# Performance work log

Hardware: AMD Instinct MI355X
Metric: run time of the kernel (lower is better)

## Reference

```python
import jax, jax.numpy as jnp
import numpy as np

N_NODES = 50000
N_EDGES = 800000
IN_DIM = 96
OUT_DIM = 96
EDGE_DIM = 32
BN_EPS = 1e-5


def setup_inputs() -> dict:
    key = jax.random.key(0)
    ks = jax.random.split(key, 12)
    x = jax.random.normal(ks[0], (N_NODES, IN_DIM), dtype=jnp.float32)
    edge_index = jax.random.randint(ks[1], (2, N_EDGES), 0, N_NODES, dtype=jnp.int64)
    edge_attr = jax.random.normal(ks[2], (N_EDGES, EDGE_DIM), dtype=jnp.float32)
    # GINEConv edge projection Linear(edge_dim, in_dim)
    We = jax.random.normal(ks[3], (EDGE_DIM, IN_DIM), dtype=jnp.float32) / np.sqrt(EDGE_DIM)
    be = jnp.zeros((IN_DIM,), dtype=jnp.float32)
    # MLP: Linear(in_dim, out_dim) -> ReLU -> Linear(out_dim, out_dim)
    W1 = jax.random.normal(ks[4], (IN_DIM, OUT_DIM), dtype=jnp.float32) / np.sqrt(IN_DIM)
    b1 = jnp.zeros((OUT_DIM,), dtype=jnp.float32)
    W2 = jax.random.normal(ks[5], (OUT_DIM, OUT_DIM), dtype=jnp.float32) / np.sqrt(OUT_DIM)
    b2 = jnp.zeros((OUT_DIM,), dtype=jnp.float32)
    # BatchNorm1d affine params
    gamma = jnp.ones((OUT_DIM,), dtype=jnp.float32)
    beta = jnp.zeros((OUT_DIM,), dtype=jnp.float32)
    return {"x": x, "edge_index": edge_index, "edge_attr": edge_attr,
            "We": We, "be": be, "W1": W1, "b1": b1, "W2": W2, "b2": b2,
            "gamma": gamma, "beta": beta}


def reference(x, edge_index, edge_attr, We, be, W1, b1, W2, b2, gamma, beta):
    src = edge_index[0]  # x_j (message source)
    dst = edge_index[1]  # aggregation target
    # GINE message: ReLU(x_j + Lin(edge_attr)) per edge  [E, in_dim]
    msg = jax.nn.relu(x[src] + edge_attr @ We + be)
    # sum aggregation into dst nodes  [N, in_dim]
    aggr = jax.ops.segment_sum(msg, dst, num_segments=x.shape[0])
    # (1 + eps) * x + aggr, eps = 0 (GINEConv default)
    h = x + aggr
    # MLP: Linear -> ReLU -> Linear
    h = jax.nn.relu(h @ W1 + b1) @ W2 + b2
    # BatchNorm1d (training-mode batch statistics) + affine
    mean = jnp.mean(h, axis=0)
    var = jnp.mean(jnp.square(h - mean), axis=0)  # biased var, as torch BN uses
    h = (h - mean) * jax.lax.rsqrt(var + BN_EPS) * gamma + beta
    # ReLU (dropout is identity in eval / deterministic reference)
    return jax.nn.relu(h)
```

## Files before the change

### kernel.cpp

```cpp
#include <hip/hip_runtime.h>

typedef unsigned short ushort_t;
typedef unsigned int uint_t;
typedef __attribute__((ext_vector_type(8))) short bf16x8;
typedef __attribute__((ext_vector_type(4))) float f32x4;
typedef __attribute__((ext_vector_type(2))) float f32x2;

#define N_NODES 50000
#define N_EDGES 800000
#define BN_EPS 1e-5f

#define OFF_STATS 4800000
#define OFF_FLAG  4801536
#define NREP 8

#define SC_PAIR  0
#define SC_LEXCL 1600000
#define SC_DEG   1650016
#define SC_RANK  1700032
#define SC_BSUM  2500032

#define NB_SCAN 196
#define MTILE 64
#define NTILES ((N_NODES + MTILE - 1) / MTILE)

__device__ __forceinline__ ushort_t f2bf(float f) {
    uint_t u = __float_as_uint(f);
    uint_t r = ((u >> 16) & 1u) + 0x7fffu;
    return (ushort_t)((u + r) >> 16);
}

__global__ __launch_bounds__(256) void init_kernel(const int* __restrict__ ei,
                                                   int* __restrict__ flag,
                                                   int* __restrict__ deg,
                                                   float* __restrict__ stats) {
    const int gtid = blockIdx.x * 256 + threadIdx.x;
    const int nth = gridDim.x * 256;
    for (int i = gtid; i < N_NODES; i += nth) deg[i] = 0;
    if (gtid < NREP * 192) stats[gtid] = 0.f;
    if (blockIdx.x == 0) {
        __shared__ int s_any;
        if (threadIdx.x == 0) s_any = 0;
        __syncthreads();
        int nz = 0;
#pragma unroll
        for (int j = 0; j < 16; ++j) {
            const int p = 1 + 2 * (threadIdx.x * 16 + j) * 195;
            if (ei[p] != 0) nz = 1;
        }
        if (nz) atomicOr(&s_any, 1);
        __syncthreads();
        if (threadIdx.x == 0) *flag = s_any ? 0 : 1;
    }
}

__global__ __launch_bounds__(256) void hist_kernel(const int* __restrict__ ei,
                                                   const int* __restrict__ flag,
                                                   int* __restrict__ deg,
                                                   int* __restrict__ rank) {
    const int is64 = *flag;
    const int stride = gridDim.x * blockDim.x;
    for (int e = blockIdx.x * blockDim.x + threadIdx.x; e < N_EDGES; e += stride) {
        int s, d;
        if (is64) { s = ei[2 * e]; d = ei[2 * N_EDGES + 2 * e]; }
        else      { s = ei[e];     d = ei[N_EDGES + e]; }
        if ((uint_t)s < N_NODES && (uint_t)d < N_NODES)
            rank[e] = atomicAdd(&deg[d], 1);
    }
}

__global__ __launch_bounds__(256) void scanA_kernel(const int* __restrict__ deg,
                                                    int* __restrict__ lexcl,
                                                    int* __restrict__ bsum) {
    __shared__ int sd[256];
    const int tid = threadIdx.x;
    const int i = blockIdx.x * 256 + tid;
    const int v = (i < N_NODES) ? deg[i] : 0;
    sd[tid] = v;
    __syncthreads();
    for (int off = 1; off < 256; off <<= 1) {
        int u = (tid >= off) ? sd[tid - off] : 0;
        __syncthreads();
        sd[tid] += u;
        __syncthreads();
    }
    if (i < N_NODES) lexcl[i] = sd[tid] - v;
    if (tid == 255) bsum[blockIdx.x] = sd[255];
}

__device__ __forceinline__ void build_sbase(const int* __restrict__ bsum,
                                            int* sd, int* sbase, int* tot) {
    const int tid = threadIdx.x;
    const int v = (tid < NB_SCAN) ? bsum[tid] : 0;
    sd[tid] = v;
    __syncthreads();
    for (int off = 1; off < 256; off <<= 1) {
        int u = (tid >= off) ? sd[tid - off] : 0;
        __syncthreads();
        sd[tid] += u;
        __syncthreads();
    }
    if (tid < NB_SCAN) sbase[tid] = sd[tid] - v;
    if (tid == NB_SCAN - 1) *tot = sd[tid];
    __syncthreads();
}

__global__ __launch_bounds__(256) void scatter_kernel(const int* __restrict__ ei,
                                                      const int* __restrict__ flag,
                                                      const int* __restrict__ lexcl,
                                                      const int* __restrict__ bsum,
                                                      const int* __restrict__ rank,
                                                      int2* __restrict__ pair) {
    __shared__ int sd[256];
    __shared__ int sbase[NB_SCAN];
    __shared__ int tot;
    build_sbase(bsum, sd, sbase, &tot);

    const int is64 = *flag;
    const int stride = gridDim.x * blockDim.x;
    for (int e = blockIdx.x * blockDim.x + threadIdx.x; e < N_EDGES; e += stride) {
        int s, d;
        if (is64) { s = ei[2 * e]; d = ei[2 * N_EDGES + 2 * e]; }
        else      { s = ei[e];     d = ei[N_EDGES + e]; }
        if ((uint_t)s < N_NODES && (uint_t)d < N_NODES) {
            const int pos = sbase[d >> 8] + lexcl[d] + rank[e];
            pair[pos] = make_int2(e, s);
        }
    }
}

__global__ __launch_bounds__(256) void node_aggr_kernel(
    const float* __restrict__ x, const float* __restrict__ ea,
    const float* __restrict__ We, const float* __restrict__ be,
    const int2* __restrict__ pair, const int* __restrict__ lexcl,
    const int* __restrict__ bsum, float* __restrict__ hbuf,
    int n0, int n1) {
    __shared__ int sd[256];
    __shared__ int sbase[NB_SCAN];
    __shared__ int tot;
    build_sbase(bsum, sd, sbase, &tot);

    const int lane = threadIdx.x & 63;
    const int q = lane >> 4;
    const int t = lane & 15;
    const int wav = blockIdx.x * 4 + (threadIdx.x >> 6);
    const int nwav = gridDim.x * 4;

    bf16x8 Bf[6];
    float ben[6];
#pragma unroll
    for (int f = 0; f < 6; ++f) {
        const int n = t + 16 * f;
#pragma unroll
        for (int j = 0; j < 8; ++j) {
            const int k = q * 8 + j;
            Bf[f][j] = (short)f2bf(We[k * 96 + n]);
        }
        ben[f] = be[n];
    }

    for (int n = n0 + wav; n < n1; n += nwav) {
        const int off = sbase[n >> 8] + lexcl[n];
        const int offn = (n + 1 == N_NODES) ? tot
                         : sbase[(n + 1) >> 8] + lexcl[n + 1];
        const int deg = offn - off;

        float part[6];
#pragma unroll
        for (int f = 0; f < 6; ++f) part[f] = 0.f;

        for (int c0 = 0; c0 < deg; c0 += 16) {
            const int rem = deg - c0;
            int eid_t = -1, src_t = -1;
            if (t < rem) {
                const int2 p = pair[off + c0 + t];
                eid_t = p.x;
                src_t = p.y;
            }
            bf16x8 A = {0, 0, 0, 0, 0, 0, 0, 0};
            if (eid_t >= 0) {
                const float* row = ea + (size_t)eid_t * 32 + q * 8;
                f32x4 a0 = *(const f32x4*)(row);
                f32x4 a1 = *(const f32x4*)(row + 4);
#pragma unroll
                for (int j = 0; j < 4; ++j) {
                    A[j] = (short)f2bf(a0[j]);
                    A[4 + j] = (short)f2bf(a1[j]);
                }
            }

            f32x4 acc[6];
#pragma unroll
            for (int f = 0; f < 6; ++f) {
                f32x4 z = {0.f, 0.f, 0.f, 0.f};
                acc[f] = __builtin_amdgcn_mfma_f32_16x16x32_bf16(A, Bf[f], z, 0, 0, 0);
            }

            int s_r[4];
#pragma unroll
            for (int r = 0; r < 4; ++r) s_r[r] = __shfl(src_t, q * 4 + r);

#pragma unroll
            for (int r = 0; r < 4; ++r) {
                const int m = q * 4 + r;
                if (m < rem) {
                    const float* xrow = x + (size_t)s_r[r] * 96;
#pragma unroll
                    for (int f = 0; f < 6; ++f) {
                        float v = acc[f][r] + ben[f] + xrow[t + 16 * f];
                        part[f] += v > 0.f ? v : 0.f;
                    }
                }
            }
        }

#pragma unroll
        for (int f = 0; f < 6; ++f) {
            part[f] += __shfl_xor(part[f], 16);
            part[f] += __shfl_xor(part[f], 32);
        }

        if (q == 0) {
            const float* xn = x + (size_t)n * 96;
            float* hn = hbuf + (size_t)n * 96;
#pragma unroll
            for (int f = 0; f < 6; ++f) {
                const int col = t + 16 * f;
                hn[col] = part[f] + xn[col];
            }
        }
    }
}

__global__ __launch_bounds__(256) void mlp_kernel(
    float* buf, const float* __restrict__ W1g, const float* __restrict__ b1g,
    const float* __restrict__ W2g, const float* __restrict__ b2g,
    float* __restrict__ stats, int tb) {
    __shared__ float Ws[96 * 96];
    __shared__ float hsT[96][68];

    const int tid = threadIdx.x;
    const int fg = tid & 15;
    const int ng = tid >> 4;
    const int n0 = (tb + blockIdx.x) * MTILE;

    for (int i = tid; i < 96 * 96 / 4; i += 256)
        ((f32x4*)Ws)[i] = ((const f32x4*)W1g)[i];
    for (int i = tid; i < MTILE * 96 / 4; i += 256) {
        const int base = i * 4;
        const int nn = base / 96, k = base - nn * 96;
        f32x4 v = {0.f, 0.f, 0.f, 0.f};
        if (n0 + nn < N_NODES)
            v = *(const f32x4*)(buf + (size_t)(n0 + nn) * 96 + k);
        hsT[k][nn] = v[0]; hsT[k + 1][nn] = v[1];
        hsT[k + 2][nn] = v[2]; hsT[k + 3][nn] = v[3];
    }
    __syncthreads();

    float acc[4][6];
#pragma unroll
    for (int ff = 0; ff < 6; ++ff) {
        const float b = b1g[6 * fg + ff];
        acc[0][ff] = b; acc[1][ff] = b; acc[2][ff] = b; acc[3][ff] = b;
    }
    for (int k = 0; k < 96; ++k) {
        const f32x4 a = *(const f32x4*)&hsT[k][4 * ng];
        const float* wr = &Ws[k * 96 + 6 * fg];
        const f32x2 w01 = *(const f32x2*)(wr);
        const f32x2 w23 = *(const f32x2*)(wr + 2);
        const f32x2 w45 = *(const f32x2*)(wr + 4);
        const float w[6] = {w01[0], w01[1], w23[0], w23[1], w45[0], w45[1]};
#pragma unroll
        for (int nn = 0; nn < 4; ++nn)
#pragma unroll
            for (int ff = 0; ff < 6; ++ff) acc[nn][ff] += a[nn] * w[ff];
    }
    __syncthreads();

#pragma unroll
    for (int nn = 0; nn < 4; ++nn)
#pragma unroll
        for (int ff = 0; ff < 6; ++ff) {
            float v = acc[nn][ff];
            hsT[6 * fg + ff][4 * ng + nn] = v > 0.f ? v : 0.f;
        }
    for (int i = tid; i < 96 * 96 / 4; i += 256)
        ((f32x4*)Ws)[i] = ((const f32x4*)W2g)[i];
    __syncthreads();

#pragma unroll
    for (int ff = 0; ff < 6; ++ff) {
        const float b = b2g[6 * fg + ff];
        acc[0][ff] = b; acc[1][ff] = b; acc[2][ff] = b; acc[3][ff] = b;
    }
    for (int k = 0; k < 96; ++k) {
        const f32x4 a = *(const f32x4*)&hsT[k][4 * ng];
        const float* wr = &Ws[k * 96 + 6 * fg];
        const f32x2 w01 = *(const f32x2*)(wr);
        const f32x2 w23 = *(const f32x2*)(wr + 2);
        const f32x2 w45 = *(const f32x2*)(wr + 4);
        const float w[6] = {w01[0], w01[1], w23[0], w23[1], w45[0], w45[1]};
#pragma unroll
        for (int nn = 0; nn < 4; ++nn)
#pragma unroll
            for (int ff = 0; ff < 6; ++ff) acc[nn][ff] += a[nn] * w[ff];
    }

#pragma unroll
    for (int nn = 0; nn < 4; ++nn) {
        const int n = n0 + 4 * ng + nn;
        if (n < N_NODES) {
            float* o = buf + (size_t)n * 96 + 6 * fg;
            *(f32x2*)(o)     = (f32x2){acc[nn][0], acc[nn][1]};
            *(f32x2*)(o + 2) = (f32x2){acc[nn][2], acc[nn][3]};
            *(f32x2*)(o + 4) = (f32x2){acc[nn][4], acc[nn][5]};
        }
    }

    __syncthreads();
#pragma unroll
    for (int nn = 0; nn < 4; ++nn)
#pragma unroll
        for (int ff = 0; ff < 6; ++ff)
            hsT[6 * fg + ff][4 * ng + nn] = acc[nn][ff];
    __syncthreads();

    if (tid < 96) {
        int nmax = N_NODES - n0;
        if (nmax > MTILE) nmax = MTILE;
        float s = 0.f, s2 = 0.f;
        for (int n = 0; n < nmax; ++n) {
            const float v = hsT[tid][n];
            s += v; s2 += v * v;
        }
        float* st = stats + (blockIdx.x & (NREP - 1)) * 192;
        atomicAdd(&st[tid], s);
        atomicAdd(&st[96 + tid], s2);
    }
}

__global__ __launch_bounds__(256) void bn_kernel(
    const float* __restrict__ h2, const float* __restrict__ stats,
    const float* __restrict__ gamma, const float* __restrict__ beta,
    float* __restrict__ out) {
    __shared__ float sc[96], sh[96];
    const int tid = threadIdx.x;
    if (tid < 96) {
        float s1 = 0.f, s2 = 0.f;
#pragma unroll
        for (int r = 0; r < NREP; ++r) {
            s1 += stats[r * 192 + tid];
            s2 += stats[r * 192 + 96 + tid];
        }
        const float inv_n = 1.f / (float)N_NODES;
        const float mean = s1 * inv_n;
        float var = s2 * inv_n - mean * mean;
        var = var > 0.f ? var : 0.f;
        const float s = gamma[tid] * rsqrtf(var + BN_EPS);
        sc[tid] = s;
        sh[tid] = beta[tid] - mean * s;
    }
    __syncthreads();
    const int total4 = N_NODES * 96 / 4;
    for (int i = blockIdx.x * blockDim.x + tid; i < total4;
         i += gridDim.x * blockDim.x) {
        f32x4 v = ((const f32x4*)h2)[i];
        const int jb = (i * 4) % 96;
#pragma unroll
        for (int c = 0; c < 4; ++c) {
            float u = v[c] * sc[jb + c] + sh[jb + c];
            v[c] = u > 0.f ? u : 0.f;
        }
        ((f32x4*)out)[i] = v;
    }
}

extern "C" void kernel_launch(void* const* d_in, const int* in_sizes, int n_in,
                              void* d_out, int out_size, void* d_ws,
                              size_t ws_size, hipStream_t stream) {
    const float* x     = (const float*)d_in[0];
    const int*   ei    = (const int*)d_in[1];
    const float* ea    = (const float*)d_in[2];
    const float* We    = (const float*)d_in[3];
    const float* be    = (const float*)d_in[4];
    const float* W1    = (const float*)d_in[5];
    const float* b1    = (const float*)d_in[6];
    const float* W2    = (const float*)d_in[7];
    const float* b2    = (const float*)d_in[8];
    const float* gamma = (const float*)d_in[9];
    const float* beta  = (const float*)d_in[10];
    float* out = (float*)d_out;

    float* ws    = (float*)d_ws;
    float* hbuf  = ws;
    float* stats = ws + OFF_STATS;
    int*   flagp = (int*)(ws + OFF_FLAG);

    int*  scratch = (int*)d_out;
    int2* pair    = (int2*)(scratch + SC_PAIR);
    int*  lexcl   = scratch + SC_LEXCL;
    int*  deg     = scratch + SC_DEG;
    int*  rank    = scratch + SC_RANK;
    int*  bsum    = scratch + SC_BSUM;

    init_kernel<<<NB_SCAN, 256, 0, stream>>>(ei, flagp, deg, stats);
    hist_kernel<<<1024, 256, 0, stream>>>(ei, flagp, deg, rank);
    scanA_kernel<<<NB_SCAN, 256, 0, stream>>>(deg, lexcl, bsum);
    scatter_kernel<<<1024, 256, 0, stream>>>(ei, flagp, lexcl, bsum, rank, pair);
    node_aggr_kernel<<<2048, 256, 0, stream>>>(x, ea, We, be, pair, lexcl,
                                               bsum, hbuf, 0, 12500);
    node_aggr_kernel<<<2048, 256, 0, stream>>>(x, ea, We, be, pair, lexcl,
                                               bsum, hbuf, 12500, 25000);
    node_aggr_kernel<<<2048, 256, 0, stream>>>(x, ea, We, be, pair, lexcl,
                                               bsum, hbuf, 25000, 37500);
    node_aggr_kernel<<<2048, 256, 0, stream>>>(x, ea, We, be, pair, lexcl,
                                               bsum, hbuf, 37500, 50000);
    mlp_kernel<<<NTILES / 2, 256, 0, stream>>>(hbuf, W1, b1, W2, b2, stats, 0);
    mlp_kernel<<<NTILES - NTILES / 2, 256, 0, stream>>>(hbuf, W1, b1, W2, b2,
                                                        stats, NTILES / 2);
    bn_kernel<<<1024, 256, 0, stream>>>(hbuf, stats, gamma, beta, out);
}
```

Before: 407.4 us.

## Process two nodes per wave in aggregation and merge split kernel launches

The node aggregation kernel now handles two destination nodes per wave at once, interleaving their edge-chunk loads and MFMAs to expose more memory-level parallelism. The four aggregation launches and two MLP launches are each merged into a single launch to cut launch overhead and tail gaps. The output write uses all 64 lanes instead of only the first 16, and the scatter writes pairs with a nontemporal 64-bit store. Pairing nodes with unequal degree wastes iterations on the shorter one and raises register pressure.

```diff
diff --git a/kernel.cpp b/kernel.cpp
--- a/kernel.cpp
+++ b/kernel.cpp
@@ -124,7 +124,9 @@
         else      { s = ei[e];     d = ei[N_EDGES + e]; }
         if ((uint_t)s < N_NODES && (uint_t)d < N_NODES) {
             const int pos = sbase[d >> 8] + lexcl[d] + rank[e];
-            pair[pos] = make_int2(e, s);
+            const unsigned long long v =
+                ((unsigned long long)(uint_t)s << 32) | (uint_t)e;
+            __builtin_nontemporal_store(v, (unsigned long long*)&pair[pos]);
         }
     }
 }
@@ -133,8 +135,7 @@
     const float* __restrict__ x, const float* __restrict__ ea,
     const float* __restrict__ We, const float* __restrict__ be,
     const int2* __restrict__ pair, const int* __restrict__ lexcl,
-    const int* __restrict__ bsum, float* __restrict__ hbuf,
-    int n0, int n1) {
+    const int* __restrict__ bsum, float* __restrict__ hbuf) {
     __shared__ int sd[256];
     __shared__ int sbase[NB_SCAN];
     __shared__ int tot;
@@ -159,74 +160,104 @@
         ben[f] = be[n];
     }
 
-    for (int n = n0 + wav; n < n1; n += nwav) {
-        const int off = sbase[n >> 8] + lexcl[n];
-        const int offn = (n + 1 == N_NODES) ? tot
-                         : sbase[(n + 1) >> 8] + lexcl[n + 1];
-        const int deg = offn - off;
-
-        float part[6];
-#pragma unroll
-        for (int f = 0; f < 6; ++f) part[f] = 0.f;
-
-        for (int c0 = 0; c0 < deg; c0 += 16) {
-            const int rem = deg - c0;
-            int eid_t = -1, src_t = -1;
-            if (t < rem) {
-                const int2 p = pair[off + c0 + t];
-                eid_t = p.x;
-                src_t = p.y;
-            }
-            bf16x8 A = {0, 0, 0, 0, 0, 0, 0, 0};
-            if (eid_t >= 0) {
-                const float* row = ea + (size_t)eid_t * 32 + q * 8;
-                f32x4 a0 = *(const f32x4*)(row);
-                f32x4 a1 = *(const f32x4*)(row + 4);
-#pragma unroll
-                for (int j = 0; j < 4; ++j) {
-                    A[j] = (short)f2bf(a0[j]);
-                    A[4 + j] = (short)f2bf(a1[j]);
+    for (int np = 2 * wav; np < N_NODES; np += 2 * nwav) {
+        int nn[2], off[2], dg[2];
+        float part[2][6];
+#pragma unroll
+        for (int s = 0; s < 2; ++s) {
+            nn[s] = np + s;
+            if (nn[s] < N_NODES) {
+                off[s] = sbase[nn[s] >> 8] + lexcl[nn[s]];
+                const int offn = (nn[s] + 1 == N_NODES)
+                                     ? tot
+                                     : sbase[(nn[s] + 1) >> 8] + lexcl[nn[s] + 1];
+                dg[s] = offn - off[s];
+            } else {
+                off[s] = 0; dg[s] = 0;
+            }
+#pragma unroll
+            for (int f = 0; f < 6; ++f) part[s][f] = 0.f;
+        }
+
+        int c[2] = {0, 0};
+        while (c[0] < dg[0] || c[1] < dg[1]) {
+            int rem[2], eid[2], src[2];
+#pragma unroll
+            for (int s = 0; s < 2; ++s) {
+                rem[s] = dg[s] - c[s];
+                eid[s] = -1; src[s] = -1;
+                if (t < rem[s]) {
+                    const int2 p = pair[off[s] + c[s] + t];
+                    eid[s] = p.x;
+                    src[s] = p.y;
                 }
             }
-
-            f32x4 acc[6];
-#pragma unroll
-            for (int f = 0; f < 6; ++f) {
-                f32x4 z = {0.f, 0.f, 0.f, 0.f};
-                acc[f] = __builtin_amdgcn_mfma_f32_16x16x32_bf16(A, Bf[f], z, 0, 0, 0);
-            }
-
-            int s_r[4];
-#pragma unroll
-            for (int r = 0; r < 4; ++r) s_r[r] = __shfl(src_t, q * 4 + r);
-
-#pragma unroll
-            for (int r = 0; r < 4; ++r) {
-                const int m = q * 4 + r;
-                if (m < rem) {
-                    const float* xrow = x + (size_t)s_r[r] * 96;
-#pragma unroll
-                    for (int f = 0; f < 6; ++f) {
-                        float v = acc[f][r] + ben[f] + xrow[t + 16 * f];
-                        part[f] += v > 0.f ? v : 0.f;
+            bf16x8 A[2];
+#pragma unroll
+            for (int s = 0; s < 2; ++s) {
+                bf16x8 a = {0, 0, 0, 0, 0, 0, 0, 0};
+                if (eid[s] >= 0) {
+                    const float* row = ea + (size_t)eid[s] * 32 + q * 8;
+                    f32x4 a0 = *(const f32x4*)(row);
+                    f32x4 a1 = *(const f32x4*)(row + 4);
+#pragma unroll
+                    for (int j = 0; j < 4; ++j) {
+                        a[j] = (short)f2bf(a0[j]);
+                        a[4 + j] = (short)f2bf(a1[j]);
                     }
                 }
-            }
-        }
-
-#pragma unroll
-        for (int f = 0; f < 6; ++f) {
-            part[f] += __shfl_xor(part[f], 16);
-            part[f] += __shfl_xor(part[f], 32);
-        }
-
-        if (q == 0) {
-            const float* xn = x + (size_t)n * 96;
-            float* hn = hbuf + (size_t)n * 96;
+                A[s] = a;
+            }
+
+            f32x4 acc[2][6];
+#pragma unroll
+            for (int s = 0; s < 2; ++s)
+#pragma unroll
+                for (int f = 0; f < 6; ++f) {
+                    f32x4 z = {0.f, 0.f, 0.f, 0.f};
+                    acc[s][f] =
+                        __builtin_amdgcn_mfma_f32_16x16x32_bf16(A[s], Bf[f], z, 0, 0, 0);
+                }
+
+#pragma unroll
+            for (int s = 0; s < 2; ++s) {
+                int s_r[4];
+#pragma unroll
+                for (int r = 0; r < 4; ++r) s_r[r] = __shfl(src[s], q * 4 + r);
+#pragma unroll
+                for (int r = 0; r < 4; ++r) {
+                    const int m = q * 4 + r;
+                    if (m < rem[s]) {
+                        const float* xrow = x + (size_t)s_r[r] * 96;
+#pragma unroll
+                        for (int f = 0; f < 6; ++f) {
+                            float v = acc[s][f][r] + ben[f] + xrow[t + 16 * f];
+                            part[s][f] += v > 0.f ? v : 0.f;
+                        }
+                    }
+                }
+            }
+            c[0] += 16;
+            c[1] += 16;
+        }
+
+#pragma unroll
+        for (int s = 0; s < 2; ++s) {
+            if (nn[s] >= N_NODES) continue;
 #pragma unroll
             for (int f = 0; f < 6; ++f) {
-                const int col = t + 16 * f;
-                hn[col] = part[f] + xn[col];
+                part[s][f] += __shfl_xor(part[s][f], 16);
+                part[s][f] += __shfl_xor(part[s][f], 32);
+            }
+            const float* xn = x + (size_t)nn[s] * 96;
+            float* hn = hbuf + (size_t)nn[s] * 96;
+            float v0 = (q == 0) ? part[s][0]
+                     : (q == 1) ? part[s][1]
+                     : (q == 2) ? part[s][2] : part[s][3];
+            hn[lane] = v0 + xn[lane];
+            if (lane < 32) {
+                float v1 = (q == 0) ? part[s][4] : part[s][5];
+                hn[64 + lane] = v1 + xn[64 + lane];
             }
         }
     }
@@ -235,14 +266,14 @@
 __global__ __launch_bounds__(256) void mlp_kernel(
     float* buf, const float* __restrict__ W1g, const float* __restrict__ b1g,
     const float* __restrict__ W2g, const float* __restrict__ b2g,
-    float* __restrict__ stats, int tb) {
+    float* __restrict__ stats) {
     __shared__ float Ws[96 * 96];
     __shared__ float hsT[96][68];
 
     const int tid = threadIdx.x;
     const int fg = tid & 15;
     const int ng = tid >> 4;
-    const int n0 = (tb + blockIdx.x) * MTILE;
+    const int n0 = blockIdx.x * MTILE;
 
     for (int i = tid; i < 96 * 96 / 4; i += 256)
         ((f32x4*)Ws)[i] = ((const f32x4*)W1g)[i];
@@ -408,15 +439,7 @@
     scanA_kernel<<<NB_SCAN, 256, 0, stream>>>(deg, lexcl, bsum);
     scatter_kernel<<<1024, 256, 0, stream>>>(ei, flagp, lexcl, bsum, rank, pair);
     node_aggr_kernel<<<2048, 256, 0, stream>>>(x, ea, We, be, pair, lexcl,
-                                               bsum, hbuf, 0, 12500);
-    node_aggr_kernel<<<2048, 256, 0, stream>>>(x, ea, We, be, pair, lexcl,
-                                               bsum, hbuf, 12500, 25000);
-    node_aggr_kernel<<<2048, 256, 0, stream>>>(x, ea, We, be, pair, lexcl,
-                                               bsum, hbuf, 25000, 37500);
-    node_aggr_kernel<<<2048, 256, 0, stream>>>(x, ea, We, be, pair, lexcl,
-                                               bsum, hbuf, 37500, 50000);
-    mlp_kernel<<<NTILES / 2, 256, 0, stream>>>(hbuf, W1, b1, W2, b2, stats, 0);
-    mlp_kernel<<<NTILES - NTILES / 2, 256, 0, stream>>>(hbuf, W1, b1, W2, b2,
-                                                        stats, NTILES / 2);
+                                               bsum, hbuf);
+    mlp_kernel<<<NTILES, 256, 0, stream>>>(hbuf, W1, b1, W2, b2, stats);
     bn_kernel<<<1024, 256, 0, stream>>>(hbuf, stats, gamma, beta, out);
 }
```

Result: slower. 416.7 us (+2.3%).
